# Kernel tuning notes

Measured on AMD Instinct MI355X. Metric: run time of the kernel, lower is better.

The kernel has to match this reference:

```python
import jax, jax.numpy as jnp
import numpy as np

DIM = 1024
HIDDEN = 4096
NUM_EXPERTS = 8
TOP_K = 2


def setup_inputs() -> dict:
    key = jax.random.key(0)
    ks = jax.random.split(key, 7)
    x = jax.random.normal(ks[0], (4, 2048, DIM), dtype=jnp.float32)
    # router Linear(dim, num_experts)
    Wr = jax.random.normal(ks[1], (DIM, NUM_EXPERTS), dtype=jnp.float32) / np.sqrt(DIM)
    br = jnp.zeros((NUM_EXPERTS,), dtype=jnp.float32)
    # stacked expert weights: Linear(dim, hidden) -> GELU -> Linear(hidden, dim)
    W1 = jax.random.normal(ks[2], (NUM_EXPERTS, DIM, HIDDEN), dtype=jnp.float32) / np.sqrt(DIM)
    b1 = jnp.zeros((NUM_EXPERTS, HIDDEN), dtype=jnp.float32)
    W2 = jax.random.normal(ks[3], (NUM_EXPERTS, HIDDEN, DIM), dtype=jnp.float32) / np.sqrt(HIDDEN)
    b2 = jnp.zeros((NUM_EXPERTS, DIM), dtype=jnp.float32)
    return {"x": x, "Wr": Wr, "br": br, "W1": W1, "b1": b1, "W2": W2, "b2": b2}


def reference(x, Wr, br, W1, b1, W2, b2):
    # router: g_x = W_e x ; p = softmax(g_x)
    logits = jnp.einsum('bsd,de->bse', x, Wr) + br            # [B,S,E]
    probs = jax.nn.softmax(logits, axis=-1)
    topk_probs, topk_idx = jax.lax.top_k(probs, TOP_K)        # [B,S,K]
    # dense compute-all-experts (faithful to torch.stack over experts)
    h = jnp.einsum('bsd,edh->bseh', x, W1) + b1               # [B,S,E,H]
    h = jax.nn.gelu(h, approximate=False)                      # torch nn.GELU default = exact erf
    expert_out = jnp.einsum('bseh,ehd->bsed', h, W2) + b2     # [B,S,E,D]
    # gather top-k expert outputs and mix
    selected = jnp.take_along_axis(expert_out, topk_idx[..., None], axis=2)  # [B,S,K,D]
    mixed = jnp.sum(topk_probs[..., None] * selected, axis=2)                # [B,S,D]
    return mixed, logits, probs, topk_idx, topk_probs
```

## Files before the change

### kernel.cpp

```cpp
#include <hip/hip_runtime.h>
#include <hip/hip_bf16.h>
#include <math.h>
#include <stdint.h>

#define DIMD 1024
#define HIDDEN 4096
#define NE 8
#define TOPK_ 2
#define T_TOKENS 8192
#define NROWS (T_TOKENS * TOPK_)
#define BK 64
#define BM1 128
#define BN1 256
#define BM2 128
#define BN2 128
#define MAXTILES (NROWS / 128 + NE)
#define TGS 8
#define NRB (T_TOKENS / 8)

typedef __bf16 bf16_t;
typedef __bf16 bf16x8 __attribute__((ext_vector_type(8)));
typedef float f32x4 __attribute__((ext_vector_type(4)));

__device__ __forceinline__ void glds16(const void* g, void* l) {
    __builtin_amdgcn_global_load_lds(
        (const __attribute__((address_space(1))) unsigned int*)g,
        (__attribute__((address_space(3))) unsigned int*)l, 16, 0, 0);
}

__device__ __forceinline__ bf16x8 ldfrag(const char* lds_, int row, int kelem) {
    int byte = row * 128 + ((kelem * 2) ^ ((row & 7) << 4));
    return *reinterpret_cast<const bf16x8*>(lds_ + byte);
}

__device__ __forceinline__ int xcd_contig(int bid, int nwg) {
    int xcd = bid & 7;
    int lid = bid >> 3;
    int q = nwg >> 3, r = nwg & 7;
    int base = (xcd < r) ? xcd * (q + 1) : r * (q + 1) + (xcd - r) * q;
    return base + lid;
}

__global__ __launch_bounds__(512) void prologue_kernel(
    const float* __restrict__ x, const float* __restrict__ Wr, const float* __restrict__ br,
    const float* __restrict__ W1, const float* __restrict__ W2,
    float* __restrict__ logits, float* __restrict__ probs,
    float* __restrict__ tidx, float* __restrict__ tprob,
    int* __restrict__ cnt, bf16_t* __restrict__ Xb,
    bf16_t* __restrict__ W1T, bf16_t* __restrict__ W2T)
{
    __shared__ float tile[128][132];
    int bid0 = blockIdx.x;
    if (bid0 < NRB) {
        int wave = threadIdx.x >> 6;
        int lane = threadIdx.x & 63;
        int t = bid0 * 8 + wave;
        const float* xr = x + (size_t)t * DIMD;
        double acc[NE];
#pragma unroll
        for (int e = 0; e < NE; ++e) acc[e] = 0.0;
        for (int i = 0; i < DIMD / 64; ++i) {
            int d = i * 64 + lane;
            double xv = (double)xr[d];
            float4 w0 = *reinterpret_cast<const float4*>(Wr + d * NE);
            float4 w1 = *reinterpret_cast<const float4*>(Wr + d * NE + 4);
            acc[0] += xv * (double)w0.x; acc[1] += xv * (double)w0.y;
            acc[2] += xv * (double)w0.z; acc[3] += xv * (double)w0.w;
            acc[4] += xv * (double)w1.x; acc[5] += xv * (double)w1.y;
            acc[6] += xv * (double)w1.z; acc[7] += xv * (double)w1.w;
        }
#pragma unroll
        for (int s = 32; s >= 1; s >>= 1) {
#pragma unroll
            for (int e = 0; e < NE; ++e) acc[e] += __shfl_xor(acc[e], s, 64);
        }
        if (lane == 0) {
            double lg[NE], mx = -1e300;
#pragma unroll
            for (int e = 0; e < NE; ++e) { lg[e] = acc[e] + (double)br[e]; mx = fmax(mx, lg[e]); }
            int i0 = 0; double l0 = -1e300;
#pragma unroll
            for (int e = 0; e < NE; ++e) { if (lg[e] > l0) { l0 = lg[e]; i0 = e; } }
            int i1 = -1; double l1 = -1e300;
#pragma unroll
            for (int e = 0; e < NE; ++e) { if (e == i0) continue; if (lg[e] > l1) { l1 = lg[e]; i1 = e; } }
            float pe[NE], s = 0.f;
#pragma unroll
            for (int e = 0; e < NE; ++e) { pe[e] = __expf((float)(lg[e] - mx)); s += pe[e]; }
            float inv = 1.f / s;
#pragma unroll
            for (int e = 0; e < NE; ++e) {
                pe[e] *= inv;
                logits[t * NE + e] = (float)lg[e];
                probs[t * NE + e] = pe[e];
            }
            tidx[t * 2 + 0] = (float)i0; tidx[t * 2 + 1] = (float)i1;
            tprob[t * 2 + 0] = pe[i0];   tprob[t * 2 + 1] = pe[i1];
            atomicAdd(&cnt[i0], 1); atomicAdd(&cnt[i1], 1);
        }
#pragma unroll
        for (int j = 0; j < 2; ++j) {
            int i = (j * 64 + lane) * 8;
            float4 a = *reinterpret_cast<const float4*>(xr + i);
            float4 b = *reinterpret_cast<const float4*>(xr + i + 4);
            bf16x8 o;
            o[0] = (bf16_t)a.x; o[1] = (bf16_t)a.y; o[2] = (bf16_t)a.z; o[3] = (bf16_t)a.w;
            o[4] = (bf16_t)b.x; o[5] = (bf16_t)b.y; o[6] = (bf16_t)b.z; o[7] = (bf16_t)b.w;
            *reinterpret_cast<bf16x8*>(Xb + (size_t)t * DIMD + i) = o;
        }
        return;
    }
    int bid = bid0 - NRB;
    const float* in; bf16_t* out; int K, N, kt, nt, e;
    if (bid < 2048) {
        in = W1; out = W1T; K = DIMD; N = HIDDEN;
        e = bid >> 8; int rem = bid & 255;
        kt = rem >> 5; nt = rem & 31;
    } else {
        bid -= 2048;
        in = W2; out = W2T; K = HIDDEN; N = DIMD;
        e = bid >> 8; int rem = bid & 255;
        kt = rem >> 3; nt = rem & 7;
    }
    int k0 = kt * 128;
    int n0 = nt * 128;
    const float* ip = in + (size_t)e * K * N + (size_t)k0 * N + n0;
    bf16_t* op = out + (size_t)e * N * K + (size_t)n0 * K + k0;
    int t = threadIdx.x;
    int r = t >> 2;
    int q = t & 3;
    const float* rp = ip + (size_t)r * N + q * 32;
#pragma unroll
    for (int i = 0; i < 8; ++i) {
        float4 v = *reinterpret_cast<const float4*>(rp + i * 4);
        *reinterpret_cast<float4*>(&tile[r][q * 32 + i * 4]) = v;
    }
    __syncthreads();
    int nn = t >> 2;
    bf16_t* wp = op + (size_t)nn * K + q * 32;
#pragma unroll
    for (int i = 0; i < 4; ++i) {
        bf16x8 o;
#pragma unroll
        for (int j = 0; j < 8; ++j) o[j] = (bf16_t)tile[q * 32 + i * 8 + j][nn];
        *reinterpret_cast<bf16x8*>(wp + i * 8) = o;
    }
}

__global__ __launch_bounds__(256) void prefix_kernel(
    const int* __restrict__ cnt, int* __restrict__ offsets,
    int* __restrict__ tileE, int* __restrict__ tileRow, int* __restrict__ numTiles)
{
    __shared__ int soff[NE + 1], scnt[NE];
    int t = threadIdx.x;
    if (t == 0) {
        int off = 0;
        for (int e = 0; e < NE; ++e) { scnt[e] = cnt[e]; soff[e] = off; off += scnt[e]; }
        soff[NE] = off;
        int nt = 0;
        for (int e = 0; e < NE; ++e) nt += (scnt[e] + 127) / 128;
        *numTiles = nt;
    }
    __syncthreads();
    if (t <= NE) offsets[t] = soff[t];
    if (t < MAXTILES) {
        int acc = 0;
#pragma unroll
        for (int e = 0; e < NE; ++e) {
            int ntE = (scnt[e] + 127) / 128;
            if (t < acc + ntE) { tileE[t] = e; tileRow[t] = soff[e] + (t - acc) * 128; return; }
            acc += ntE;
        }
    }
}

__global__ __launch_bounds__(256) void scatter_kernel(
    const float* __restrict__ tidx, const float* __restrict__ tprob,
    const int* __restrict__ offsets, int* __restrict__ gcursor,
    int* __restrict__ rowToken, int* __restrict__ tokRow)
{
    __shared__ int lcnt[NE], lbase[NE];
    int t = blockIdx.x * 256 + threadIdx.x;
    if (threadIdx.x < NE) lcnt[threadIdx.x] = 0;
    __syncthreads();
    int e0 = (int)tidx[t * 2 + 0], e1 = (int)tidx[t * 2 + 1];
    int r0l = atomicAdd(&lcnt[e0], 1);
    int r1l = atomicAdd(&lcnt[e1], 1);
    __syncthreads();
    if (threadIdx.x < NE) lbase[threadIdx.x] = atomicAdd(&gcursor[threadIdx.x], lcnt[threadIdx.x]);
    __syncthreads();
    int r0 = offsets[e0] + lbase[e0] + r0l;
    int r1 = offsets[e1] + lbase[e1] + r1l;
    rowToken[r0] = t; rowToken[r1] = t;
    tokRow[t * 2 + 0] = r0; tokRow[t * 2 + 1] = r1;
}

__global__ __launch_bounds__(512) void ffn1_kernel(
    const bf16_t* __restrict__ Xb, const bf16_t* __restrict__ W1T, const float* __restrict__ b1,
    const int* __restrict__ tileE, const int* __restrict__ tileRow, const int* __restrict__ numTiles,
    const int* __restrict__ offsets, const int* __restrict__ rowToken,
    bf16_t* __restrict__ h)
{
    const int NB = HIDDEN / BN1;
    int logical = xcd_contig(blockIdx.x, gridDim.x);
    int tg  = logical / (NB * TGS);
    int rem = logical % (NB * TGS);
    int nb  = rem / TGS;
    int ti  = rem % TGS;
    int tile = tg * TGS + ti;
    if (tile >= *numTiles) return;
    int e = tileE[tile];
    int row0 = tileRow[tile];
    int rend = offsets[e + 1];
    int n0 = nb * BN1;

    __shared__ __align__(16) char lds[49152];

    int tid = threadIdx.x;
    int lane = tid & 63;
    int wid = tid >> 6;
    int wr = (wid >> 2) * 64;
    int wc = (wid & 3) * 64;
    int rr = lane & 15;
    int k4 = (lane >> 4) * 8;

    int srow = tid >> 3;
    int xc = (((tid & 7) ^ (srow & 7)) << 4);
    const char *pa0, *pa1, *pb0, *pb1, *pb2, *pb3;
    {
        int g0 = row0 + srow;      if (g0 > NROWS - 1) g0 = NROWS - 1;
        int g1 = row0 + 64 + srow; if (g1 > NROWS - 1) g1 = NROWS - 1;
        pa0 = (const char*)(Xb + (size_t)rowToken[g0] * DIMD) + xc;
        pa1 = (const char*)(Xb + (size_t)rowToken[g1] * DIMD) + xc;
        pb0 = (const char*)(W1T + ((size_t)e * HIDDEN + n0 + srow) * DIMD) + xc;
        pb1 = (const char*)(W1T + ((size_t)e * HIDDEN + n0 + 64 + srow) * DIMD) + xc;
        pb2 = (const char*)(W1T + ((size_t)e * HIDDEN + n0 + 128 + srow) * DIMD) + xc;
        pb3 = (const char*)(W1T + ((size_t)e * HIDDEN + n0 + 192 + srow) * DIMD) + xc;
    }

    f32x4 acc[4][4];
#pragma unroll
    for (int i = 0; i < 4; ++i)
#pragma unroll
        for (int j = 0; j < 4; ++j) acc[i][j] = f32x4{0.f, 0.f, 0.f, 0.f};

    for (int t_ = 0; t_ < DIMD / BK; ++t_) {
        int kb = t_ * 128;
        glds16(pa0 + kb, lds + wid * 1024);
        glds16(pa1 + kb, lds + 8192 + wid * 1024);
        glds16(pb0 + kb, lds + 16384 + wid * 1024);
        glds16(pb1 + kb, lds + 24576 + wid * 1024);
        glds16(pb2 + kb, lds + 32768 + wid * 1024);
        glds16(pb3 + kb, lds + 40960 + wid * 1024);
        __syncthreads();
#pragma unroll
        for (int ks = 0; ks < 2; ++ks) {
            int kk = ks * 32 + k4;
            bf16x8 b_[4], a_[4];
#pragma unroll
            for (int n = 0; n < 4; ++n) b_[n] = ldfrag(lds + 16384, wc + n * 16 + rr, kk);
#pragma unroll
            for (int m = 0; m < 4; ++m) a_[m] = ldfrag(lds, wr + m * 16 + rr, kk);
#pragma unroll
            for (int m = 0; m < 4; ++m)
#pragma unroll
                for (int n = 0; n < 4; ++n)
                    acc[m][n] = __builtin_amdgcn_mfma_f32_16x16x32_bf16(a_[m], b_[n], acc[m][n], 0, 0, 0);
        }
        __syncthreads();
    }

    int crow = (lane >> 4) * 4;
    int ccol = lane & 15;
#pragma unroll
    for (int m = 0; m < 4; ++m) {
#pragma unroll
        for (int n = 0; n < 4; ++n) {
            int col = wc + n * 16 + ccol;
            float bias = b1[e * HIDDEN + n0 + col];
#pragma unroll
            for (int r = 0; r < 4; ++r) {
                int row = row0 + wr + m * 16 + crow + r;
                if (row < rend) {
                    float v = acc[m][n][r] + bias;
                    float g = 0.5f * v * (1.0f + erff(v * 0.70710678118654752f));
                    h[(size_t)row * HIDDEN + n0 + col] = (bf16_t)g;
                }
            }
        }
    }
}

__global__ __launch_bounds__(256) void ffn2_kernel(
    const bf16_t* __restrict__ h, const bf16_t* __restrict__ W2T, const float* __restrict__ b2,
    const int* __restrict__ tileE, const int* __restrict__ tileRow, const int* __restrict__ numTiles,
    const int* __restrict__ offsets, float* __restrict__ part)
{
    const int NB = DIMD / BN2;
    int logical = xcd_contig(blockIdx.x, gridDim.x);
    int tile = logical / NB;
    int nb = logical % NB;
    if (tile >= *numTiles) return;
    int e = tileE[tile];
    int row0 = tileRow[tile];
    int rend = offsets[e + 1];
    int n0 = nb * BN2;

    __shared__ __align__(16) char lds[32768];

    int tid = threadIdx.x;
    int lane = tid & 63;
    int wid = tid >> 6;
    int wr = (wid >> 1) * 64;
    int wc = (wid & 1) * 64;
    int rr = lane & 15;
    int k4 = (lane >> 4) * 8;

    int srow = tid >> 3;
    int xc = (((tid & 7) ^ (srow & 7)) << 4);
    const char *pa0, *pa1, *pa2, *pa3, *pb0, *pb1, *pb2, *pb3;
    {
        int g0 = row0 + srow;      if (g0 > NROWS - 1) g0 = NROWS - 1;
        int g1 = row0 + 32 + srow; if (g1 > NROWS - 1) g1 = NROWS - 1;
        int g2 = row0 + 64 + srow; if (g2 > NROWS - 1) g2 = NROWS - 1;
        int g3 = row0 + 96 + srow; if (g3 > NROWS - 1) g3 = NROWS - 1;
        pa0 = (const char*)(h + (size_t)g0 * HIDDEN) + xc;
        pa1 = (const char*)(h + (size_t)g1 * HIDDEN) + xc;
        pa2 = (const char*)(h + (size_t)g2 * HIDDEN) + xc;
        pa3 = (const char*)(h + (size_t)g3 * HIDDEN) + xc;
        pb0 = (const char*)(W2T + ((size_t)e * DIMD + n0 + srow) * HIDDEN) + xc;
        pb1 = (const char*)(W2T + ((size_t)e * DIMD + n0 + 32 + srow) * HIDDEN) + xc;
        pb2 = (const char*)(W2T + ((size_t)e * DIMD + n0 + 64 + srow) * HIDDEN) + xc;
        pb3 = (const char*)(W2T + ((size_t)e * DIMD + n0 + 96 + srow) * HIDDEN) + xc;
    }

    f32x4 acc[4][4];
#pragma unroll
    for (int i = 0; i < 4; ++i)
#pragma unroll
        for (int j = 0; j < 4; ++j) acc[i][j] = f32x4{0.f, 0.f, 0.f, 0.f};

    for (int t_ = 0; t_ < HIDDEN / BK; ++t_) {
        int kb = t_ * 128;
        char* dA = lds + wid * 1024;
        char* dB = lds + 16384 + wid * 1024;
        glds16(pa0 + kb, dA);          glds16(pb0 + kb, dB);
        glds16(pa1 + kb, dA + 4096);   glds16(pb1 + kb, dB + 4096);
        glds16(pa2 + kb, dA + 8192);   glds16(pb2 + kb, dB + 8192);
        glds16(pa3 + kb, dA + 12288);  glds16(pb3 + kb, dB + 12288);
        __syncthreads();
#pragma unroll
        for (int ks = 0; ks < 2; ++ks) {
            int kk = ks * 32 + k4;
            bf16x8 a_[4], b_[4];
#pragma unroll
            for (int m = 0; m < 4; ++m) a_[m] = ldfrag(lds, wr + m * 16 + rr, kk);
#pragma unroll
            for (int n = 0; n < 4; ++n) b_[n] = ldfrag(lds + 16384, wc + n * 16 + rr, kk);
#pragma unroll
            for (int m = 0; m < 4; ++m)
#pragma unroll
                for (int n = 0; n < 4; ++n)
                    acc[m][n] = __builtin_amdgcn_mfma_f32_16x16x32_bf16(a_[m], b_[n], acc[m][n], 0, 0, 0);
        }
        __syncthreads();
    }

    int crow = (lane >> 4) * 4;
    int ccol = lane & 15;
#pragma unroll
    for (int m = 0; m < 4; ++m) {
#pragma unroll
        for (int n = 0; n < 4; ++n) {
            int col = wc + n * 16 + ccol;
            int dcol = n0 + col;
            float bias = b2[e * DIMD + dcol];
#pragma unroll
            for (int r = 0; r < 4; ++r) {
                int row = row0 + wr + m * 16 + crow + r;
                if (row < rend) {
                    part[(size_t)row * DIMD + dcol] = acc[m][n][r] + bias;
                }
            }
        }
    }
}

__global__ __launch_bounds__(256) void reduce_kernel(
    const float* __restrict__ part, const float* __restrict__ tprob,
    const int* __restrict__ tokRow, float* __restrict__ mixed)
{
    int idx = blockIdx.x * 256 + threadIdx.x;
    int tok = idx >> 8;
    int q = (idx & 255) * 4;
    int r0 = tokRow[tok * 2 + 0], r1 = tokRow[tok * 2 + 1];
    float p0 = tprob[tok * 2 + 0], p1 = tprob[tok * 2 + 1];
    float4 a = *reinterpret_cast<const float4*>(part + (size_t)r0 * DIMD + q);
    float4 b = *reinterpret_cast<const float4*>(part + (size_t)r1 * DIMD + q);
    float4 o;
    o.x = p0 * a.x + p1 * b.x;
    o.y = p0 * a.y + p1 * b.y;
    o.z = p0 * a.z + p1 * b.z;
    o.w = p0 * a.w + p1 * b.w;
    *reinterpret_cast<float4*>(mixed + (size_t)tok * DIMD + q) = o;
}

extern "C" void kernel_launch(void* const* d_in, const int* in_sizes, int n_in,
                              void* d_out, int out_size, void* d_ws, size_t ws_size,
                              hipStream_t stream)
{
    const float* x  = (const float*)d_in[0];
    const float* Wr = (const float*)d_in[1];
    const float* br = (const float*)d_in[2];
    const float* W1 = (const float*)d_in[3];
    const float* b1 = (const float*)d_in[4];
    const float* W2 = (const float*)d_in[5];
    const float* b2 = (const float*)d_in[6];

    float* out = (float*)d_out;
    float* mixed  = out;
    float* logits = out + (size_t)T_TOKENS * DIMD;
    float* probs  = logits + T_TOKENS * NE;
    float* tidx   = probs + T_TOKENS * NE;
    float* tprob  = tidx + T_TOKENS * TOPK_;

    char* p = (char*)d_ws;
    auto alloc = [&](size_t bytes) { char* r = p; p += (bytes + 255) & ~255ull; return r; };
    int*    small    = (int*)alloc(2 * NE * 4);
    int*    cnt      = small;
    int*    gcursor  = small + NE;
    int*    offsets  = (int*)alloc((NE + 1) * 4);
    int*    numTiles = (int*)alloc(4);
    int*    tileE    = (int*)alloc(MAXTILES * 4);
    int*    tileRow  = (int*)alloc(MAXTILES * 4);
    int*    rowToken = (int*)alloc(NROWS * 4);
    int*    tokRow   = (int*)alloc(NROWS * 4);
    bf16_t* W1T      = (bf16_t*)alloc((size_t)NE * HIDDEN * DIMD * 2);
    bf16_t* W2T      = (bf16_t*)alloc((size_t)NE * DIMD * HIDDEN * 2);
    bf16_t* Xb       = (bf16_t*)alloc((size_t)T_TOKENS * DIMD * 2);
    bf16_t* hbuf     = (bf16_t*)alloc((size_t)NROWS * HIDDEN * 2);
    float*  part     = (float*)alloc((size_t)NROWS * DIMD * 4);

    hipMemsetAsync(small, 0, 2 * NE * 4, stream);

    prologue_kernel<<<NRB + 4096, 512, 0, stream>>>(
        x, Wr, br, W1, W2, logits, probs, tidx, tprob, cnt, Xb, W1T, W2T);
    prefix_kernel<<<1, 256, 0, stream>>>(cnt, offsets, tileE, tileRow, numTiles);
    scatter_kernel<<<T_TOKENS / 256, 256, 0, stream>>>(tidx, tprob, offsets, gcursor, rowToken, tokRow);

    ffn1_kernel<<<MAXTILES * (HIDDEN / BN1), 512, 0, stream>>>(
        Xb, W1T, b1, tileE, tileRow, numTiles, offsets, rowToken, hbuf);
    ffn2_kernel<<<MAXTILES * (DIMD / BN2), 256, 0, stream>>>(
        hbuf, W2T, b2, tileE, tileRow, numTiles, offsets, part);
    reduce_kernel<<<T_TOKENS * DIMD / 4 / 256, 256, 0, stream>>>(part, tprob, tokRow, mixed);
}
```

Measured before the change: 717.1 us.

## Move W2 transpose into ffn1 launch and use bf16 LDS transpose tiles

The W2 fp32-to-bf16 transpose moves out of the prologue kernel and into extra leading blocks of the ffn1 launch, so it can overlap with the grouped GEMM instead of sitting on the critical path before routing. The shared transpose helper now converts to bf16 before writing LDS, which halves the LDS tile footprint and store traffic. The cost is a larger ffn1 grid whose first blocks do different work, which may perturb the XCD tile mapping and occupancy of the GEMM blocks.

```diff
diff --git a/kernel.cpp b/kernel.cpp
--- a/kernel.cpp
+++ b/kernel.cpp
@@ -17,6 +17,7 @@
 #define MAXTILES (NROWS / 128 + NE)
 #define TGS 8
 #define NRB (T_TOKENS / 8)
+#define NW2T 2048
 
 typedef __bf16 bf16_t;
 typedef __bf16 bf16x8 __attribute__((ext_vector_type(8)));
@@ -41,15 +42,49 @@
     return base + lid;
 }
 
+__device__ __forceinline__ void transpose_tile(
+    const float* __restrict__ in, bf16_t* __restrict__ out,
+    int K, int N, int kt, int nt, char* ldsraw)
+{
+    bf16_t (*tile)[136] = reinterpret_cast<bf16_t(*)[136]>(ldsraw);
+    int k0 = kt * 128, n0 = nt * 128;
+    const float* ip = in + (size_t)k0 * N + n0;
+    bf16_t* op = out + (size_t)n0 * K + k0;
+    int t = threadIdx.x;
+    int r = t >> 2;
+    int q = t & 3;
+    const float* rp = ip + (size_t)r * N + q * 32;
+    bf16_t* trow = &tile[r][q * 32];
+#pragma unroll
+    for (int i = 0; i < 4; ++i) {
+        float4 a = *reinterpret_cast<const float4*>(rp + i * 8);
+        float4 b = *reinterpret_cast<const float4*>(rp + i * 8 + 4);
+        bf16x8 o;
+        o[0] = (bf16_t)a.x; o[1] = (bf16_t)a.y; o[2] = (bf16_t)a.z; o[3] = (bf16_t)a.w;
+        o[4] = (bf16_t)b.x; o[5] = (bf16_t)b.y; o[6] = (bf16_t)b.z; o[7] = (bf16_t)b.w;
+        *reinterpret_cast<bf16x8*>(trow + i * 8) = o;
+    }
+    __syncthreads();
+    int nn = t >> 2;
+    bf16_t* wp = op + (size_t)nn * K + q * 32;
+#pragma unroll
+    for (int i = 0; i < 4; ++i) {
+        bf16x8 o;
+#pragma unroll
+        for (int j = 0; j < 8; ++j) o[j] = tile[q * 32 + i * 8 + j][nn];
+        *reinterpret_cast<bf16x8*>(wp + i * 8) = o;
+    }
+}
+
 __global__ __launch_bounds__(512) void prologue_kernel(
     const float* __restrict__ x, const float* __restrict__ Wr, const float* __restrict__ br,
-    const float* __restrict__ W1, const float* __restrict__ W2,
+    const float* __restrict__ W1,
     float* __restrict__ logits, float* __restrict__ probs,
     float* __restrict__ tidx, float* __restrict__ tprob,
     int* __restrict__ cnt, bf16_t* __restrict__ Xb,
-    bf16_t* __restrict__ W1T, bf16_t* __restrict__ W2T)
-{
-    __shared__ float tile[128][132];
+    bf16_t* __restrict__ W1T)
+{
+    __shared__ __align__(16) char ldsraw[34816];
     int bid0 = blockIdx.x;
     if (bid0 < NRB) {
         int wave = threadIdx.x >> 6;
@@ -111,40 +146,11 @@
         return;
     }
     int bid = bid0 - NRB;
-    const float* in; bf16_t* out; int K, N, kt, nt, e;
-    if (bid < 2048) {
-        in = W1; out = W1T; K = DIMD; N = HIDDEN;
-        e = bid >> 8; int rem = bid & 255;
-        kt = rem >> 5; nt = rem & 31;
-    } else {
-        bid -= 2048;
-        in = W2; out = W2T; K = HIDDEN; N = DIMD;
-        e = bid >> 8; int rem = bid & 255;
-        kt = rem >> 3; nt = rem & 7;
-    }
-    int k0 = kt * 128;
-    int n0 = nt * 128;
-    const float* ip = in + (size_t)e * K * N + (size_t)k0 * N + n0;
-    bf16_t* op = out + (size_t)e * N * K + (size_t)n0 * K + k0;
-    int t = threadIdx.x;
-    int r = t >> 2;
-    int q = t & 3;
-    const float* rp = ip + (size_t)r * N + q * 32;
-#pragma unroll
-    for (int i = 0; i < 8; ++i) {
-        float4 v = *reinterpret_cast<const float4*>(rp + i * 4);
-        *reinterpret_cast<float4*>(&tile[r][q * 32 + i * 4]) = v;
-    }
-    __syncthreads();
-    int nn = t >> 2;
-    bf16_t* wp = op + (size_t)nn * K + q * 32;
-#pragma unroll
-    for (int i = 0; i < 4; ++i) {
-        bf16x8 o;
-#pragma unroll
-        for (int j = 0; j < 8; ++j) o[j] = (bf16_t)tile[q * 32 + i * 8 + j][nn];
-        *reinterpret_cast<bf16x8*>(wp + i * 8) = o;
-    }
+    int e = bid >> 8;
+    int rem = bid & 255;
+    int kt = rem >> 5, nt = rem & 31;
+    transpose_tile(W1 + (size_t)e * DIMD * HIDDEN, W1T + (size_t)e * HIDDEN * DIMD,
+                   DIMD, HIDDEN, kt, nt, ldsraw);
 }
 
 __global__ __launch_bounds__(256) void prefix_kernel(
@@ -197,12 +203,23 @@
 
 __global__ __launch_bounds__(512) void ffn1_kernel(
     const bf16_t* __restrict__ Xb, const bf16_t* __restrict__ W1T, const float* __restrict__ b1,
+    const float* __restrict__ W2, bf16_t* __restrict__ W2T,
     const int* __restrict__ tileE, const int* __restrict__ tileRow, const int* __restrict__ numTiles,
     const int* __restrict__ offsets, const int* __restrict__ rowToken,
     bf16_t* __restrict__ h)
 {
+    __shared__ __align__(16) char lds[49152];
+    int bid0 = blockIdx.x;
+    if (bid0 < NW2T) {
+        int e = bid0 >> 8;
+        int rem = bid0 & 255;
+        int kt = rem >> 3, nt = rem & 7;
+        transpose_tile(W2 + (size_t)e * HIDDEN * DIMD, W2T + (size_t)e * DIMD * HIDDEN,
+                       HIDDEN, DIMD, kt, nt, lds);
+        return;
+    }
     const int NB = HIDDEN / BN1;
-    int logical = xcd_contig(blockIdx.x, gridDim.x);
+    int logical = xcd_contig(bid0 - NW2T, gridDim.x - NW2T);
     int tg  = logical / (NB * TGS);
     int rem = logical % (NB * TGS);
     int nb  = rem / TGS;
@@ -213,8 +230,6 @@
     int row0 = tileRow[tile];
     int rend = offsets[e + 1];
     int n0 = nb * BN1;
-
-    __shared__ __align__(16) char lds[49152];
 
     int tid = threadIdx.x;
     int lane = tid & 63;
@@ -443,13 +458,13 @@
 
     hipMemsetAsync(small, 0, 2 * NE * 4, stream);
 
-    prologue_kernel<<<NRB + 4096, 512, 0, stream>>>(
-        x, Wr, br, W1, W2, logits, probs, tidx, tprob, cnt, Xb, W1T, W2T);
+    prologue_kernel<<<NRB + 2048, 512, 0, stream>>>(
+        x, Wr, br, W1, logits, probs, tidx, tprob, cnt, Xb, W1T);
     prefix_kernel<<<1, 256, 0, stream>>>(cnt, offsets, tileE, tileRow, numTiles);
     scatter_kernel<<<T_TOKENS / 256, 256, 0, stream>>>(tidx, tprob, offsets, gcursor, rowToken, tokRow);
 
-    ffn1_kernel<<<MAXTILES * (HIDDEN / BN1), 512, 0, stream>>>(
-        Xb, W1T, b1, tileE, tileRow, numTiles, offsets, rowToken, hbuf);
+    ffn1_kernel<<<NW2T + MAXTILES * (HIDDEN / BN1), 512, 0, stream>>>(
+        Xb, W1T, b1, W2, W2T, tileE, tileRow, numTiles, offsets, rowToken, hbuf);
     ffn2_kernel<<<MAXTILES * (DIMD / BN2), 256, 0, stream>>>(
         hbuf, W2T, b2, tileE, tileRow, numTiles, offsets, part);
     reduce_kernel<<<T_TOKENS * DIMD / 4 / 256, 256, 0, stream>>>(part, tprob, tokRow, mixed);
```

Result: no change. 730.2 us (+1.8%).
